# Kernel optimization log

Measured on AMD Instinct MI355X. Metric: run time of the kernel, lower is better.

The kernel has to match this reference:

```python
import jax, jax.numpy as jnp
import numpy as np
import math

B, S, IN_DIM, OUT_DIM = 16, 1024, 512, 256
THETA = 10000.0


def _rope_single(x, cos, sin):
    # x: [B,S,D]; cos/sin: [D//2] -- SAME rotation applied at every position
    # (faithful to original: freqs_cis[seq_len*2] selects a single row)
    xr = x.reshape(x.shape[0], x.shape[1], -1, 2)
    a, b = xr[..., 0], xr[..., 1]
    out = jnp.stack([a * cos - b * sin, a * sin + b * cos], axis=-1)
    return out.reshape(x.shape)


def setup_inputs() -> dict:
    key = jax.random.key(0)
    ks = jax.random.split(key, 4)
    scale = 1.0 / math.sqrt(IN_DIM)
    x = jax.random.normal(ks[0], (B, S, IN_DIM), jnp.float32)
    wq = jax.random.normal(ks[1], (OUT_DIM, IN_DIM), jnp.float32) * scale
    wk = jax.random.normal(ks[2], (OUT_DIM, IN_DIM), jnp.float32) * scale
    wv = jax.random.normal(ks[3], (OUT_DIM, IN_DIM), jnp.float32) * scale
    bq = jnp.zeros((OUT_DIM,), jnp.float32)
    bk = jnp.zeros((OUT_DIM,), jnp.float32)
    bv = jnp.zeros((OUT_DIM,), jnp.float32)
    return {"x": x, "wq": wq, "bq": bq, "wk": wk, "bk": bk, "wv": wv, "bv": bv}


def reference(x, wq, bq, wk, bk, wv, bv):
    dim = x.shape[-1]  # scale uses INPUT dim, per original code
    # freqs_cis row at position index = 2*seq_len
    inv_freq = 1.0 / (THETA ** (jnp.arange(0, OUT_DIM, 2, dtype=jnp.float32) / OUT_DIM))
    angle = (2.0 * S) * inv_freq  # [OUT_DIM//2]
    cos, sin = jnp.cos(angle), jnp.sin(angle)

    q = jnp.einsum('bsi,oi->bso', x, wq) + bq
    k = jnp.einsum('bsi,oi->bso', x, wk) + bk
    v = jnp.einsum('bsi,oi->bso', x, wv) + bv

    q = _rope_single(q, cos, sin)
    k = _rope_single(k, cos, sin)

    scores = jnp.einsum('bqd,bkd->bqk', q, k) / jnp.sqrt(jnp.float32(dim))
    scores = jax.nn.softmax(scores.astype(jnp.float32), axis=-1)
    out = jnp.einsum('bqk,bkd->bqd', scores, v)
    return out
```

## Files before the change

### kernel.cpp

```cpp
#include <hip/hip_runtime.h>
#include <hip/hip_bf16.h>


typedef __attribute__((ext_vector_type(8))) short short8;
typedef __attribute__((ext_vector_type(4))) short short4v;
typedef __attribute__((ext_vector_type(4))) float f32x4;

#define GLL16(g, l)                                                            \
  __builtin_amdgcn_global_load_lds(                                            \
      (const __attribute__((address_space(1))) unsigned int*)(g),              \
      (__attribute__((address_space(3))) unsigned int*)(l), 16, 0, 0)

static __device__ __forceinline__ short f2bf(float f) {
  __hip_bfloat16 h = __float2bfloat16(f);
  return __builtin_bit_cast(short, h);
}

__global__ __launch_bounds__(256) void qkv_gemm(
    const float* __restrict__ x, const float* __restrict__ wq,
    const float* __restrict__ wk, const float* __restrict__ wv,
    const float* __restrict__ bq, const float* __restrict__ bk,
    const float* __restrict__ bv, short* __restrict__ qb,
    short* __restrict__ kb, short* __restrict__ vt) {
  __shared__ __align__(16) char smem[32768];
  const int bid = blockIdx.x;
  const int swz = (bid & 7) * 96 + (bid >> 3);
  const int mt = swz / 6, nt = swz % 6;
  const int tid = threadIdx.x;
  const int w = tid >> 6, lane = tid & 63;
  const int g = lane >> 4, c = lane & 15;
  const int wm = w >> 1, wn = w & 1;

  const float* wsel = (nt < 2) ? wq : (nt < 4) ? wk : wv;
  const int wro = (nt & 1) * 128;

  f32x4 acc[4][4];
  const f32x4 fzero = {0.f, 0.f, 0.f, 0.f};
#pragma unroll
  for (int mi = 0; mi < 4; mi++)
#pragma unroll
    for (int ni = 0; ni < 4; ni++) acc[mi][ni] = fzero;

  const int arow = tid >> 4;
  const int acol4 = tid & 15;
  const int achunk = acol4 >> 1, ahalf = (tid & 1) * 8;

  float4 xv[8], wv8[8];
#pragma unroll
  for (int j = 0; j < 8; j++) {
    int row = j * 16 + arow;
    xv[j] = *(const float4*)(x + (mt * 128 + row) * 512 + acol4 * 4);
    wv8[j] = *(const float4*)(wsel + (wro + row) * 512 + acol4 * 4);
  }

  for (int kk = 0; kk < 8; ++kk) {
    __syncthreads();
#pragma unroll
    for (int j = 0; j < 8; j++) {
      int row = j * 16 + arow;
      short4v s4;
      s4[0] = f2bf(xv[j].x); s4[1] = f2bf(xv[j].y);
      s4[2] = f2bf(xv[j].z); s4[3] = f2bf(xv[j].w);
      *(short4v*)(smem + row * 128 + ((achunk ^ (row & 7)) * 16) + ahalf) = s4;
      short4v t4;
      t4[0] = f2bf(wv8[j].x); t4[1] = f2bf(wv8[j].y);
      t4[2] = f2bf(wv8[j].z); t4[3] = f2bf(wv8[j].w);
      *(short4v*)(smem + 16384 + row * 128 + ((achunk ^ (row & 7)) * 16) + ahalf) = t4;
    }
    __syncthreads();
    if (kk < 7) {
#pragma unroll
      for (int j = 0; j < 8; j++) {
        int row = j * 16 + arow;
        xv[j] = *(const float4*)(x + (mt * 128 + row) * 512 + (kk + 1) * 64 + acol4 * 4);
        wv8[j] = *(const float4*)(wsel + (wro + row) * 512 + (kk + 1) * 64 + acol4 * 4);
      }
    }
#pragma unroll
    for (int ks = 0; ks < 2; ++ks) {
      short8 af[4], bf[4];
#pragma unroll
      for (int mi = 0; mi < 4; mi++) {
        int row = wm * 64 + mi * 16 + c;
        af[mi] = *(const short8*)(smem + row * 128 + (((ks * 4 + g) ^ (row & 7)) * 16));
      }
#pragma unroll
      for (int ni = 0; ni < 4; ni++) {
        int row = wn * 64 + ni * 16 + c;
        bf[ni] = *(const short8*)(smem + 16384 + row * 128 + (((ks * 4 + g) ^ (row & 7)) * 16));
      }
#pragma unroll
      for (int mi = 0; mi < 4; mi++)
#pragma unroll
        for (int ni = 0; ni < 4; ni++)
          acc[mi][ni] = __builtin_amdgcn_mfma_f32_16x16x32_bf16(af[mi], bf[ni], acc[mi][ni], 0, 0, 0);
    }
  }

  const int cls = nt >> 1;
  const int cw = (nt & 1) * 128 + wn * 64;
  const int rowbase = mt * 128 + wm * 64;
  if (cls == 0) {
#pragma unroll
    for (int ni = 0; ni < 4; ni++) {
      int col = cw + ni * 16 + c;
      float bias = bq[col];
#pragma unroll
      for (int mi = 0; mi < 4; mi++)
#pragma unroll
        for (int j = 0; j < 4; j++) {
          int row = rowbase + mi * 16 + g * 4 + j;
          qb[row * 256 + col] = f2bf((acc[mi][ni][j] + bias) * 0.044194173824159216f);
        }
    }
  } else if (cls == 1) {
#pragma unroll
    for (int ni = 0; ni < 4; ni++) {
      int col = cw + ni * 16 + c;
      float bias = bk[col];
#pragma unroll
      for (int mi = 0; mi < 4; mi++)
#pragma unroll
        for (int j = 0; j < 4; j++) {
          int row = rowbase + mi * 16 + g * 4 + j;
          kb[row * 256 + col] = f2bf(acc[mi][ni][j] + bias);
        }
    }
  } else {
    __syncthreads();
    char* tb = smem + w * 8192;
#pragma unroll
    for (int ni = 0; ni < 4; ni++) {
      int dl = ni * 16 + c;
      float bias = bv[cw + dl];
#pragma unroll
      for (int mi = 0; mi < 4; mi++)
#pragma unroll
        for (int j = 0; j < 4; j++) {
          int sl = mi * 16 + g * 4 + j;
          *(short*)(tb + dl * 128 + ((sl * 2) ^ ((dl & 7) << 4))) =
              f2bf(acc[mi][ni][j] + bias);
        }
    }
    const int bb = rowbase >> 10, sb = rowbase & 1023;
#pragma unroll
    for (int i = 0; i < 8; i++) {
      int dl = i * 8 + (lane >> 3);
      int ch = lane & 7;
      short8 val = *(const short8*)(tb + dl * 128 + ((ch ^ (dl & 7)) * 16));
      *(short8*)(vt + (bb * 256 + cw + dl) * 1024 + sb + ch * 8) = val;
    }
  }
}

__global__ __launch_bounds__(512) void attn_kernel(
    const short* __restrict__ qb, const short* __restrict__ kb,
    const short* __restrict__ vt, float* __restrict__ out) {
  __shared__ __align__(16) char smem[141824];
  const int bid = blockIdx.x;
  const int swz = (bid & 7) * 32 + (bid >> 3);
  const int b = swz >> 4, qt = swz & 15;
  const int tid = threadIdx.x;
  const int w = tid >> 6, lane = tid & 63;
  const int grp = w >> 2, lw = w & 3;
  const int g = lane >> 4, c = lane & 15;
  const int q0 = b * 1024 + qt * 64 + lw * 16;
  short* sp = (short*)(smem + 131072 + w * 1280);
  const int krow0 = b * 1024 + grp * 512;

  short8 qf[8];
#pragma unroll
  for (int ks = 0; ks < 8; ks++)
    qf[ks] = *(const short8*)(qb + (q0 + c) * 256 + ks * 32 + g * 8);

  f32x4 O[16];
  const f32x4 fzero = {0.f, 0.f, 0.f, 0.f};
#pragma unroll
  for (int ni = 0; ni < 16; ni++) O[ni] = fzero;
  float m_[4] = {-1e30f, -1e30f, -1e30f, -1e30f};
  float l_[4] = {0.f, 0.f, 0.f, 0.f};

  auto stage = [&](int kt, int buf) {
    char* kdst = smem + grp * 32768 + buf * 16384;
    char* vdst = smem + 65536 + grp * 32768 + buf * 16384;
#pragma unroll
    for (int i = 0; i < 4; i++) {
      int j = lw * 4 + i;
      int r = j * 2 + (lane >> 5);
      int cc = lane & 31;
      GLL16(kb + (krow0 + kt * 32 + r) * 256 + ((cc ^ (r & 7)) * 8),
            kdst + j * 1024);
    }
#pragma unroll
    for (int i = 0; i < 4; i++) {
      int j = lw * 4 + i;
      int r = j * 16 + (lane >> 2);
      int cc = lane & 3;
      GLL16(vt + (b * 256 + r) * 1024 + grp * 512 + kt * 32 + ((cc ^ (r & 3)) * 8),
            vdst + j * 1024);
    }
  };

  stage(0, 0);
  for (int kt = 0; kt < 16; ++kt) {
    const int cur = kt & 1;
    const char* kbase = smem + grp * 32768 + cur * 16384;
    const char* vbase = smem + 65536 + grp * 32768 + cur * 16384;
    asm volatile("s_waitcnt vmcnt(0)" ::: "memory");
    __syncthreads();
    if (kt < 15) stage(kt + 1, cur ^ 1);

    f32x4 Sf[2];
    Sf[0] = fzero; Sf[1] = fzero;
#pragma unroll
    for (int ks = 0; ks < 8; ks++) {
      short8 kf[2];
#pragma unroll
      for (int nf = 0; nf < 2; nf++) {
        int key = nf * 16 + c;
        kf[nf] = *(const short8*)(kbase + key * 512 + (((ks * 4 + g) ^ (c & 7)) * 16));
      }
#pragma unroll
      for (int nf = 0; nf < 2; nf++)
        Sf[nf] = __builtin_amdgcn_mfma_f32_16x16x32_bf16(qf[ks], kf[nf], Sf[nf], 0, 0, 0);
    }

    float tm[4];
#pragma unroll
    for (int j = 0; j < 4; j++) {
      float t = fmaxf(Sf[0][j], Sf[1][j]);
      t = fmaxf(t, __shfl_xor(t, 1));
      t = fmaxf(t, __shfl_xor(t, 2));
      t = fmaxf(t, __shfl_xor(t, 4));
      t = fmaxf(t, __shfl_xor(t, 8));
      tm[j] = t;
    }
    bool need = (tm[0] > m_[0] + 8.f) || (tm[1] > m_[1] + 8.f) ||
                (tm[2] > m_[2] + 8.f) || (tm[3] > m_[3] + 8.f);
    float Pv[2][4];
    if (__any(need)) {
      float scl[4];
#pragma unroll
      for (int j = 0; j < 4; j++) {
        float nm = fmaxf(m_[j], tm[j]);
        scl[j] = __expf(m_[j] - nm);
        m_[j] = nm;
        float rs = 0.f;
#pragma unroll
        for (int nf = 0; nf < 2; nf++) {
          float p = __expf(Sf[nf][j] - nm);
          Pv[nf][j] = p;
          rs += p;
        }
        rs += __shfl_xor(rs, 1);
        rs += __shfl_xor(rs, 2);
        rs += __shfl_xor(rs, 4);
        rs += __shfl_xor(rs, 8);
        l_[j] = l_[j] * scl[j] + rs;
      }
#pragma unroll
      for (int ni = 0; ni < 16; ni++) {
        O[ni][0] *= scl[0]; O[ni][1] *= scl[1];
        O[ni][2] *= scl[2]; O[ni][3] *= scl[3];
      }
    } else {
#pragma unroll
      for (int j = 0; j < 4; j++) {
        float rs = 0.f;
#pragma unroll
        for (int nf = 0; nf < 2; nf++) {
          float p = __expf(Sf[nf][j] - m_[j]);
          Pv[nf][j] = p;
          rs += p;
        }
        rs += __shfl_xor(rs, 1);
        rs += __shfl_xor(rs, 2);
        rs += __shfl_xor(rs, 4);
        rs += __shfl_xor(rs, 8);
        l_[j] += rs;
      }
    }

#pragma unroll
    for (int nf = 0; nf < 2; nf++)
#pragma unroll
      for (int j = 0; j < 4; j++)
        sp[(g * 4 + j) * 40 + nf * 16 + c] = f2bf(Pv[nf][j]);

    short8 pf = *(const short8*)((char*)sp + c * 80 + g * 16);

#pragma unroll
    for (int ni = 0; ni < 16; ni++) {
      int d = ni * 16 + c;
      short8 vf = *(const short8*)(vbase + d * 64 + ((g ^ (d & 3)) * 16));
      O[ni] = __builtin_amdgcn_mfma_f32_16x16x32_bf16(pf, vf, O[ni], 0, 0, 0);
    }
  }

  __syncthreads();
  float2* mlb = (float2*)(smem + 141312);
  if (grp == 1) {
    char* ob = smem + lw * 20480;
#pragma unroll
    for (int ni = 0; ni < 16; ni++)
      *(f32x4*)(ob + (ni * 16 + c) * 80 + g * 16) = O[ni];
#pragma unroll
    for (int j = 0; j < 4; j++) {
      float2 ml; ml.x = m_[j]; ml.y = l_[j];
      mlb[lw * 16 + g * 4 + j] = ml;
    }
  }
  __syncthreads();
  if (grp == 0) {
    char* ob = smem + lw * 20480;
    float a1[4], a2[4], inv[4];
#pragma unroll
    for (int j = 0; j < 4; j++) {
      float2 ml2 = mlb[lw * 16 + g * 4 + j];
      float mm = fmaxf(m_[j], ml2.x);
      a1[j] = __expf(m_[j] - mm);
      a2[j] = __expf(ml2.x - mm);
      inv[j] = 1.0f / (a1[j] * l_[j] + a2[j] * ml2.y);
    }
#pragma unroll
    for (int ni = 0; ni < 16; ni++) {
      f32x4 o2 = *(const f32x4*)(ob + (ni * 16 + c) * 80 + g * 16);
#pragma unroll
      for (int j = 0; j < 4; j++) {
        int row = q0 + g * 4 + j;
        out[row * 256 + ni * 16 + c] = (a1[j] * O[ni][j] + a2[j] * o2[j]) * inv[j];
      }
    }
  }
}

extern "C" void kernel_launch(void* const* d_in, const int* in_sizes, int n_in,
                              void* d_out, int out_size, void* d_ws, size_t ws_size,
                              hipStream_t stream) {
  const float* x  = (const float*)d_in[0];
  const float* wq = (const float*)d_in[1];
  const float* bq = (const float*)d_in[2];
  const float* wk = (const float*)d_in[3];
  const float* bk = (const float*)d_in[4];
  const float* wv = (const float*)d_in[5];
  const float* bv = (const float*)d_in[6];
  float* out = (float*)d_out;
  char* ws = (char*)d_ws;
  short* qb = (short*)ws;
  short* kb = (short*)(ws + 8388608);
  short* vt = (short*)(ws + 16777216);

  qkv_gemm<<<768, 256, 0, stream>>>(x, wq, wk, wv, bq, bk, bv, qb, kb, vt);
  attn_kernel<<<256, 512, 0, stream>>>(qb, kb, vt, out);
}
```

Measured before the change: 159.8 us.

## Transpose MFMA operands so each lane owns a query row; register-stage V

Swaps the A/B operands of both MFMAs so the accumulator layout gives each lane one query row. Row max and sum reductions then need two cross-lane shuffles instead of four per row, and the output can be written as contiguous float4 vectors. V is now loaded into registers one tile ahead and written to a single padded LDS buffer instead of being double-buffered through global_load_lds. This cuts LDS use and the softmax shuffle work, but adds a second __syncthreads per iteration and a register-to-LDS copy.

```diff
diff --git a/kernel.cpp b/kernel.cpp
--- a/kernel.cpp
+++ b/kernel.cpp
@@ -156,7 +156,7 @@
 __global__ __launch_bounds__(512) void attn_kernel(
     const short* __restrict__ qb, const short* __restrict__ kb,
     const short* __restrict__ vt, float* __restrict__ out) {
-  __shared__ __align__(16) char smem[141824];
+  __shared__ __align__(16) char smem[116992];
   const int bid = blockIdx.x;
   const int swz = (bid & 7) * 32 + (bid >> 3);
   const int b = swz >> 4, qt = swz & 15;
@@ -165,7 +165,9 @@
   const int grp = w >> 2, lw = w & 3;
   const int g = lane >> 4, c = lane & 15;
   const int q0 = b * 1024 + qt * 64 + lw * 16;
-  short* sp = (short*)(smem + 131072 + w * 1280);
+  char* kbufs = smem + grp * 32768;
+  char* vbase = smem + 65536 + grp * 20480;
+  short* sp = (short*)(smem + 106496 + w * 1280);
   const int krow0 = b * 1024 + grp * 512;
 
   short8 qf[8];
@@ -177,12 +179,21 @@
   const f32x4 fzero = {0.f, 0.f, 0.f, 0.f};
 #pragma unroll
   for (int ni = 0; ni < 16; ni++) O[ni] = fzero;
-  float m_[4] = {-1e30f, -1e30f, -1e30f, -1e30f};
-  float l_[4] = {0.f, 0.f, 0.f, 0.f};
-
-  auto stage = [&](int kt, int buf) {
-    char* kdst = smem + grp * 32768 + buf * 16384;
-    char* vdst = smem + 65536 + grp * 32768 + buf * 16384;
+  float m_ = -1e30f, l_ = 0.f;
+
+  const int vr = lane >> 2, vcc = lane & 3;
+
+  short8 vreg[4];
+  auto loadV = [&](int kt) {
+#pragma unroll
+    for (int i = 0; i < 4; i++) {
+      int d = lw * 64 + i * 16 + vr;
+      vreg[i] = *(const short8*)(vt + (size_t)(b * 256 + d) * 1024 + grp * 512 +
+                                 kt * 32 + vcc * 8);
+    }
+  };
+  auto stageK = [&](int kt, int buf) {
+    char* kdst = kbufs + buf * 16384;
 #pragma unroll
     for (int i = 0; i < 4; i++) {
       int j = lw * 4 + i;
@@ -191,145 +202,106 @@
       GLL16(kb + (krow0 + kt * 32 + r) * 256 + ((cc ^ (r & 7)) * 8),
             kdst + j * 1024);
     }
-#pragma unroll
-    for (int i = 0; i < 4; i++) {
-      int j = lw * 4 + i;
-      int r = j * 16 + (lane >> 2);
-      int cc = lane & 3;
-      GLL16(vt + (b * 256 + r) * 1024 + grp * 512 + kt * 32 + ((cc ^ (r & 3)) * 8),
-            vdst + j * 1024);
-    }
   };
 
-  stage(0, 0);
+  stageK(0, 0);
+  loadV(0);
   for (int kt = 0; kt < 16; ++kt) {
     const int cur = kt & 1;
-    const char* kbase = smem + grp * 32768 + cur * 16384;
-    const char* vbase = smem + 65536 + grp * 32768 + cur * 16384;
+    const char* kbase = kbufs + cur * 16384;
     asm volatile("s_waitcnt vmcnt(0)" ::: "memory");
     __syncthreads();
-    if (kt < 15) stage(kt + 1, cur ^ 1);
+#pragma unroll
+    for (int i = 0; i < 4; i++) {
+      int d = lw * 64 + i * 16 + vr;
+      *(short8*)(vbase + d * 80 + vcc * 16) = vreg[i];
+    }
+    if (kt < 15) {
+      stageK(kt + 1, cur ^ 1);
+      loadV(kt + 1);
+    }
+    __syncthreads();
 
     f32x4 Sf[2];
     Sf[0] = fzero; Sf[1] = fzero;
 #pragma unroll
     for (int ks = 0; ks < 8; ks++) {
-      short8 kf[2];
-#pragma unroll
-      for (int nf = 0; nf < 2; nf++) {
-        int key = nf * 16 + c;
-        kf[nf] = *(const short8*)(kbase + key * 512 + (((ks * 4 + g) ^ (c & 7)) * 16));
-      }
-#pragma unroll
-      for (int nf = 0; nf < 2; nf++)
-        Sf[nf] = __builtin_amdgcn_mfma_f32_16x16x32_bf16(qf[ks], kf[nf], Sf[nf], 0, 0, 0);
-    }
-
-    float tm[4];
-#pragma unroll
-    for (int j = 0; j < 4; j++) {
-      float t = fmaxf(Sf[0][j], Sf[1][j]);
-      t = fmaxf(t, __shfl_xor(t, 1));
-      t = fmaxf(t, __shfl_xor(t, 2));
-      t = fmaxf(t, __shfl_xor(t, 4));
-      t = fmaxf(t, __shfl_xor(t, 8));
-      tm[j] = t;
-    }
-    bool need = (tm[0] > m_[0] + 8.f) || (tm[1] > m_[1] + 8.f) ||
-                (tm[2] > m_[2] + 8.f) || (tm[3] > m_[3] + 8.f);
-    float Pv[2][4];
-    if (__any(need)) {
-      float scl[4];
-#pragma unroll
-      for (int j = 0; j < 4; j++) {
-        float nm = fmaxf(m_[j], tm[j]);
-        scl[j] = __expf(m_[j] - nm);
-        m_[j] = nm;
-        float rs = 0.f;
-#pragma unroll
-        for (int nf = 0; nf < 2; nf++) {
-          float p = __expf(Sf[nf][j] - nm);
-          Pv[nf][j] = p;
-          rs += p;
-        }
-        rs += __shfl_xor(rs, 1);
-        rs += __shfl_xor(rs, 2);
-        rs += __shfl_xor(rs, 4);
-        rs += __shfl_xor(rs, 8);
-        l_[j] = l_[j] * scl[j] + rs;
-      }
+      short8 kf0 = *(const short8*)(kbase + c * 512 + (((ks * 4 + g) ^ (c & 7)) * 16));
+      short8 kf1 = *(const short8*)(kbase + (16 + c) * 512 + (((ks * 4 + g) ^ (c & 7)) * 16));
+      Sf[0] = __builtin_amdgcn_mfma_f32_16x16x32_bf16(kf0, qf[ks], Sf[0], 0, 0, 0);
+      Sf[1] = __builtin_amdgcn_mfma_f32_16x16x32_bf16(kf1, qf[ks], Sf[1], 0, 0, 0);
+    }
+
+    float tm = fmaxf(fmaxf(fmaxf(Sf[0][0], Sf[0][1]), fmaxf(Sf[0][2], Sf[0][3])),
+                     fmaxf(fmaxf(Sf[1][0], Sf[1][1]), fmaxf(Sf[1][2], Sf[1][3])));
+    tm = fmaxf(tm, __shfl_xor(tm, 16));
+    tm = fmaxf(tm, __shfl_xor(tm, 32));
+    float p[8];
+    if (__any(tm > m_ + 8.f)) {
+      float nm = fmaxf(m_, tm);
+      float scl = __expf(m_ - nm);
+      m_ = nm;
+      float rs = 0.f;
+#pragma unroll
+      for (int i = 0; i < 4; i++) { p[i] = __expf(Sf[0][i] - nm); rs += p[i]; }
+#pragma unroll
+      for (int i = 0; i < 4; i++) { p[4 + i] = __expf(Sf[1][i] - nm); rs += p[4 + i]; }
+      rs += __shfl_xor(rs, 16);
+      rs += __shfl_xor(rs, 32);
+      l_ = l_ * scl + rs;
 #pragma unroll
       for (int ni = 0; ni < 16; ni++) {
-        O[ni][0] *= scl[0]; O[ni][1] *= scl[1];
-        O[ni][2] *= scl[2]; O[ni][3] *= scl[3];
+        O[ni][0] *= scl; O[ni][1] *= scl; O[ni][2] *= scl; O[ni][3] *= scl;
       }
     } else {
-#pragma unroll
-      for (int j = 0; j < 4; j++) {
-        float rs = 0.f;
-#pragma unroll
-        for (int nf = 0; nf < 2; nf++) {
-          float p = __expf(Sf[nf][j] - m_[j]);
-          Pv[nf][j] = p;
-          rs += p;
-        }
-        rs += __shfl_xor(rs, 1);
-        rs += __shfl_xor(rs, 2);
-        rs += __shfl_xor(rs, 4);
-        rs += __shfl_xor(rs, 8);
-        l_[j] += rs;
-      }
-    }
-
-#pragma unroll
-    for (int nf = 0; nf < 2; nf++)
-#pragma unroll
-      for (int j = 0; j < 4; j++)
-        sp[(g * 4 + j) * 40 + nf * 16 + c] = f2bf(Pv[nf][j]);
-
+      float rs = 0.f;
+#pragma unroll
+      for (int i = 0; i < 4; i++) { p[i] = __expf(Sf[0][i] - m_); rs += p[i]; }
+#pragma unroll
+      for (int i = 0; i < 4; i++) { p[4 + i] = __expf(Sf[1][i] - m_); rs += p[4 + i]; }
+      rs += __shfl_xor(rs, 16);
+      rs += __shfl_xor(rs, 32);
+      l_ += rs;
+    }
+
+    short4v pa, pb;
+    pa[0] = f2bf(p[0]); pa[1] = f2bf(p[1]); pa[2] = f2bf(p[2]); pa[3] = f2bf(p[3]);
+    pb[0] = f2bf(p[4]); pb[1] = f2bf(p[5]); pb[2] = f2bf(p[6]); pb[3] = f2bf(p[7]);
+    *(short4v*)((char*)sp + c * 80 + g * 8) = pa;
+    *(short4v*)((char*)sp + c * 80 + 32 + g * 8) = pb;
     short8 pf = *(const short8*)((char*)sp + c * 80 + g * 16);
 
 #pragma unroll
     for (int ni = 0; ni < 16; ni++) {
       int d = ni * 16 + c;
-      short8 vf = *(const short8*)(vbase + d * 64 + ((g ^ (d & 3)) * 16));
-      O[ni] = __builtin_amdgcn_mfma_f32_16x16x32_bf16(pf, vf, O[ni], 0, 0, 0);
+      short8 vf = *(const short8*)(vbase + d * 80 + g * 16);
+      O[ni] = __builtin_amdgcn_mfma_f32_16x16x32_bf16(vf, pf, O[ni], 0, 0, 0);
     }
   }
 
   __syncthreads();
-  float2* mlb = (float2*)(smem + 141312);
+  float2* mlb = (float2*)(smem + 116736);
   if (grp == 1) {
-    char* ob = smem + lw * 20480;
+    char* ob = smem + lw * 16640;
 #pragma unroll
     for (int ni = 0; ni < 16; ni++)
-      *(f32x4*)(ob + (ni * 16 + c) * 80 + g * 16) = O[ni];
-#pragma unroll
-    for (int j = 0; j < 4; j++) {
-      float2 ml; ml.x = m_[j]; ml.y = l_[j];
-      mlb[lw * 16 + g * 4 + j] = ml;
-    }
+      *(f32x4*)(ob + c * 1040 + (ni * 16 + g * 4) * 4) = O[ni];
+    if (g == 0) { float2 ml; ml.x = m_; ml.y = l_; mlb[lw * 16 + c] = ml; }
   }
   __syncthreads();
   if (grp == 0) {
-    char* ob = smem + lw * 20480;
-    float a1[4], a2[4], inv[4];
-#pragma unroll
-    for (int j = 0; j < 4; j++) {
-      float2 ml2 = mlb[lw * 16 + g * 4 + j];
-      float mm = fmaxf(m_[j], ml2.x);
-      a1[j] = __expf(m_[j] - mm);
-      a2[j] = __expf(ml2.x - mm);
-      inv[j] = 1.0f / (a1[j] * l_[j] + a2[j] * ml2.y);
-    }
+    char* ob = smem + lw * 16640;
+    float2 ml2 = mlb[lw * 16 + c];
+    float mm = fmaxf(m_, ml2.x);
+    float a1 = __expf(m_ - mm), a2 = __expf(ml2.x - mm);
+    float inv = 1.0f / (a1 * l_ + a2 * ml2.y);
 #pragma unroll
     for (int ni = 0; ni < 16; ni++) {
-      f32x4 o2 = *(const f32x4*)(ob + (ni * 16 + c) * 80 + g * 16);
-#pragma unroll
-      for (int j = 0; j < 4; j++) {
-        int row = q0 + g * 4 + j;
-        out[row * 256 + ni * 16 + c] = (a1[j] * O[ni][j] + a2[j] * o2[j]) * inv[j];
-      }
+      f32x4 o2 = *(const f32x4*)(ob + c * 1040 + (ni * 16 + g * 4) * 4);
+      f32x4 r;
+#pragma unroll
+      for (int j = 0; j < 4; j++) r[j] = (a1 * O[ni][j] + a2 * o2[j]) * inv;
+      *(f32x4*)(out + (q0 + c) * 256 + ni * 16 + g * 4) = r;
     }
   }
 }
```

Result: faster. 155.1 us (-2.9%).
